# Optimization experiments

Hardware: AMD Instinct MI355X
Metric: run time of the kernel (lower is better)

The kernel has to match this reference:

```python
import math
import jax, jax.numpy as jnp
import numpy as np

B, L, D, H = 4, 2048, 1024, 16
KD = D // H

def setup_inputs() -> dict:
    key = jax.random.key(0)
    k1, k2, k3 = jax.random.split(key, 3)
    x = jax.random.normal(k1, (B, L, D), dtype=jnp.float32)
    pad_mask = jnp.zeros((B, L), dtype=bool)  # True = padded (masked) key position
    w_qkv = jax.random.normal(k2, (D, 3 * D), dtype=jnp.float32) / math.sqrt(D)
    w_out = jax.random.normal(k3, (D, D), dtype=jnp.float32) / math.sqrt(D)
    return {"x": x, "pad_mask": pad_mask, "w_qkv": w_qkv, "w_out": w_out}

def reference(x, pad_mask, w_qkv, w_out):
    Bx, Lx, Dx = x.shape
    qkv = jnp.einsum('bld,de->ble', x, w_qkv)          # [B,L,3D]
    q, k, v = jnp.split(qkv, 3, axis=-1)
    def heads(t):
        return t.reshape(Bx, Lx, H, KD).transpose(0, 2, 1, 3)  # [B,H,L,kd]
    qh, kh, vh = heads(q), heads(k), heads(v)
    scores = jnp.einsum('bhqd,bhkd->bhqk', qh, kh) / math.sqrt(KD)
    causal = jnp.triu(jnp.ones((Lx, Lx), dtype=bool), k=1)[None, None]   # [1,1,L,L]
    mask = causal | pad_mask[:, None, None, :]                            # [B,1,L,L]
    scores = jnp.where(mask, -jnp.inf, scores)
    probs = jax.nn.softmax(scores, axis=-1)
    att = jnp.einsum('bhqk,bhkd->bhqd', probs, vh)
    concat = att.transpose(0, 2, 1, 3).reshape(Bx, Lx, Dx)
    return jnp.einsum('bld,de->ble', concat, w_out)
```

## Files before the change

### kernel.cpp

```cpp
#include <hip/hip_runtime.h>
#include <hip/hip_bf16.h>
#include <math.h>


typedef __bf16 bf16x8 __attribute__((ext_vector_type(8)));
typedef float f32x4 __attribute__((ext_vector_type(4)));

__device__ __forceinline__ f32x4 mfma16(bf16x8 a, bf16x8 b, f32x4 c) {
    return __builtin_amdgcn_mfma_f32_16x16x32_bf16(a, b, c, 0, 0, 0);
}

__device__ __forceinline__ void async16(const void* g, void* l) {
    __builtin_amdgcn_global_load_lds(
        (const __attribute__((address_space(1))) unsigned int*)g,
        (__attribute__((address_space(3))) unsigned int*)l, 16, 0, 0);
}

__global__ void prologue(const float* __restrict__ x,
                         __hip_bfloat16* __restrict__ xb,
                         const float* __restrict__ w0,
                         __hip_bfloat16* __restrict__ t0,
                         const float* __restrict__ w1,
                         __hip_bfloat16* __restrict__ t1) {
    __shared__ float tile[32][33];
    int bid = blockIdx.x, tid = threadIdx.x;
    if (bid < 8192) {
        int i = bid * 256 + tid;
        float4 v = ((const float4*)x)[i];
        __hip_bfloat16 t[4];
        t[0] = __float2bfloat16(v.x);
        t[1] = __float2bfloat16(v.y);
        t[2] = __float2bfloat16(v.z);
        t[3] = __float2bfloat16(v.w);
        ((uint2*)xb)[i] = *(uint2*)t;
        return;
    }
    int t = bid - 8192;
    const float* W;
    __hip_bfloat16* Wt;
    int N, bx, by;
    if (t < 3072) { W = w0; Wt = t0; N = 3072; bx = t % 96; by = t / 96; }
    else { t -= 3072; W = w1; Wt = t1; N = 1024; bx = t % 32; by = t / 32; }
    const int K = 1024;
    int tx = tid & 31, ty = tid >> 5;
    int n0 = bx * 32, k0 = by * 32;
#pragma unroll
    for (int i = 0; i < 4; ++i)
        tile[ty + 8 * i][tx] = W[(size_t)(k0 + ty + 8 * i) * N + n0 + tx];
    __syncthreads();
#pragma unroll
    for (int i = 0; i < 4; ++i)
        Wt[(size_t)(n0 + ty + 8 * i) * K + k0 + tx] =
            __float2bfloat16(tile[tx][ty + 8 * i]);
}

__global__ __launch_bounds__(256) void gemm_qkv(
    const __hip_bfloat16* __restrict__ A, const __hip_bfloat16* __restrict__ Bt,
    __hip_bfloat16* __restrict__ Qo, __hip_bfloat16* __restrict__ Ko,
    __hip_bfloat16* __restrict__ Vto, int M, int N, int K) {
    __shared__ __hip_bfloat16 As[128 * 64];
    __shared__ __hip_bfloat16 Bs[128 * 64];
    int tid = threadIdx.x;
    int wave = tid >> 6, lane = tid & 63;
    int quad = lane >> 4, l16 = lane & 15;
    int m0 = blockIdx.x * 128, n0 = blockIdx.y * 128;
    int wm = (wave >> 1) * 64, wn = (wave & 1) * 64;
    int srow = lane >> 3;
    int g8 = ((lane & 7) ^ srow) * 8;
    int swz = (l16 & 7);
    f32x4 acc[4][4] = {};
    for (int k0 = 0; k0 < K; k0 += 64) {
        __syncthreads();
#pragma unroll
        for (int j = 0; j < 4; ++j) {
            int r0 = (j * 4 + wave) * 8;
            async16(&A[(size_t)(m0 + r0 + srow) * K + k0 + g8], &As[r0 * 64]);
            async16(&Bt[(size_t)(n0 + r0 + srow) * K + k0 + g8], &Bs[r0 * 64]);
        }
        __syncthreads();
        bf16x8 af[2][4], bfr[2][4];
#pragma unroll
        for (int c = 0; c < 2; ++c) {
            int pg = ((c * 4 + quad) ^ swz) * 8;
#pragma unroll
            for (int i = 0; i < 4; ++i) {
                af[c][i]  = *(const bf16x8*)&As[(wm + i * 16 + l16) * 64 + pg];
                bfr[c][i] = *(const bf16x8*)&Bs[(wn + i * 16 + l16) * 64 + pg];
            }
        }
#pragma unroll
        for (int c = 0; c < 2; ++c)
#pragma unroll
            for (int mi = 0; mi < 4; ++mi)
#pragma unroll
                for (int ni = 0; ni < 4; ++ni)
                    acc[mi][ni] = mfma16(af[c][mi], bfr[c][ni], acc[mi][ni]);
    }
#pragma unroll
    for (int mi = 0; mi < 4; ++mi) {
#pragma unroll
        for (int ni = 0; ni < 4; ++ni) {
            int row0 = m0 + wm + mi * 16 + quad * 4;
            int col = n0 + wn + ni * 16 + l16;
            int which = col >> 10, hd = col & 1023;
            int h = hd >> 6, d = hd & 63;
            if (which == 0) {
#pragma unroll
                for (int r = 0; r < 4; ++r) {
                    int row = row0 + r;
                    int b = row >> 11, l = row & 2047;
                    Qo[(((size_t)b * 16 + h) * 2048 + l) * 64 + d] =
                        __float2bfloat16(acc[mi][ni][r] * 0.18033688011f);
                }
            } else if (which == 1) {
#pragma unroll
                for (int r = 0; r < 4; ++r) {
                    int row = row0 + r;
                    int b = row >> 11, l = row & 2047;
                    Ko[(((size_t)b * 16 + h) * 2048 + l) * 64 + d] =
                        __float2bfloat16(acc[mi][ni][r]);
                }
            } else {
                int b = row0 >> 11, l = row0 & 2047;
                __hip_bfloat16 t4[4];
#pragma unroll
                for (int r = 0; r < 4; ++r)
                    t4[r] = __float2bfloat16(acc[mi][ni][r]);
                *(uint2*)&Vto[(((size_t)b * 16 + h) * 64 + d) * 2048 + l] =
                    *(uint2*)t4;
            }
        }
    }
}

__global__ __launch_bounds__(256) void gemm_out(
    const __hip_bfloat16* __restrict__ A, const __hip_bfloat16* __restrict__ Bt,
    float* __restrict__ Cf, int M, int N, int K) {
    __shared__ __hip_bfloat16 As[2][128 * 64];
    __shared__ __hip_bfloat16 Bs[2][64 * 64];
    int tid = threadIdx.x;
    int wave = tid >> 6, lane = tid & 63;
    int quad = lane >> 4, l16 = lane & 15;
    int m0 = blockIdx.x * 128, n0 = blockIdx.y * 64;
    int wm = wave * 32;
    int srow = lane >> 3;
    int g8 = ((lane & 7) ^ srow) * 8;
    int swz = (l16 & 7);

    auto stage = [&](int k0, int buf) {
#pragma unroll
        for (int j = 0; j < 4; ++j) {
            int r0 = (wave * 4 + j) * 8;
            async16(&A[(size_t)(m0 + r0 + srow) * K + k0 + g8],
                    &As[buf][r0 * 64]);
        }
#pragma unroll
        for (int j = 0; j < 2; ++j) {
            int r0 = (wave * 2 + j) * 8;
            async16(&Bt[(size_t)(n0 + r0 + srow) * K + k0 + g8],
                    &Bs[buf][r0 * 64]);
        }
    };

    f32x4 acc[2][4] = {};
    int niter = K >> 6;
    stage(0, 0);
    for (int kt = 0; kt < niter; ++kt) {
        int cur = kt & 1;
        __syncthreads();
        if (kt + 1 < niter) stage((kt + 1) * 64, cur ^ 1);
        bf16x8 af[2][2], bfr[2][4];
#pragma unroll
        for (int c = 0; c < 2; ++c) {
            int pg = ((c * 4 + quad) ^ swz) * 8;
#pragma unroll
            for (int i = 0; i < 2; ++i)
                af[c][i] =
                    *(const bf16x8*)&As[cur][(wm + i * 16 + l16) * 64 + pg];
#pragma unroll
            for (int i = 0; i < 4; ++i)
                bfr[c][i] = *(const bf16x8*)&Bs[cur][(i * 16 + l16) * 64 + pg];
        }
#pragma unroll
        for (int c = 0; c < 2; ++c)
#pragma unroll
            for (int mi = 0; mi < 2; ++mi)
#pragma unroll
                for (int ni = 0; ni < 4; ++ni)
                    acc[mi][ni] = mfma16(af[c][mi], bfr[c][ni], acc[mi][ni]);
    }
#pragma unroll
    for (int mi = 0; mi < 2; ++mi)
#pragma unroll
        for (int ni = 0; ni < 4; ++ni) {
            int row0 = m0 + wm + mi * 16 + quad * 4;
            int col = n0 + ni * 16 + l16;
#pragma unroll
            for (int r = 0; r < 4; ++r)
                Cf[(size_t)(row0 + r) * N + col] = acc[mi][ni][r];
        }
}

__global__ __launch_bounds__(256, 2) void attn_kernel(
    const __hip_bfloat16* __restrict__ Q, const __hip_bfloat16* __restrict__ Kk,
    const __hip_bfloat16* __restrict__ Vt,
    const unsigned char* __restrict__ pm, __hip_bfloat16* __restrict__ Ao) {
    __shared__ __hip_bfloat16 Ks[2 * 64 * 64];
    __shared__ __hip_bfloat16 Vs[2 * 64 * 64];
    constexpr int LDK = 72;
    __shared__ __hip_bfloat16 Ps[4 * 32 * LDK];
    __shared__ unsigned char pmS[2048];
    __shared__ unsigned char pmAny[32];
    int tid = threadIdx.x;
    int wave = tid >> 6, lane = tid & 63;
    int quad = lane >> 4, l16 = lane & 15;
    int srow = lane >> 3;
    int g8 = ((lane & 7) ^ srow) * 8;
    int swz = (l16 & 7);
    int lin = blockIdx.x;
    int bh = (lin & 7) * 8 + ((lin >> 3) & 7);
    int pr = lin >> 6;
    int b = bh >> 4, h = bh & 15;
    const __hip_bfloat16* Qbh = Q + (size_t)bh * 2048 * 64;
    const __hip_bfloat16* Kbh = Kk + (size_t)bh * 2048 * 64;
    const __hip_bfloat16* Vbh = Vt + (size_t)bh * 64 * 2048;
    *(uint2*)&pmS[tid * 8] = *(const uint2*)&pm[b * 2048 + tid * 8];
    __syncthreads();
    if (tid < 32) {
        const unsigned long long* q8 = (const unsigned long long*)&pmS[tid * 64];
        unsigned long long v = q8[0] | q8[1] | q8[2] | q8[3] | q8[4] | q8[5] |
                               q8[6] | q8[7];
        pmAny[tid] = v ? 1 : 0;
    }
    __hip_bfloat16* Pw = Ps + wave * 32 * LDK;

    auto stage = [&](int kt, int buf) {
#pragma unroll
        for (int j = 0; j < 2; ++j) {
            int r0 = (j * 4 + wave) * 8;
            async16(&Kbh[((size_t)kt * 64 + r0 + srow) * 64 + g8],
                    &Ks[buf * 4096 + r0 * 64]);
            async16(&Vbh[(size_t)(r0 + srow) * 2048 + kt * 64 + g8],
                    &Vs[buf * 4096 + r0 * 64]);
        }
    };

#pragma unroll
    for (int ph = 0; ph < 2; ++ph) {
        int qt = ph ? pr : 15 - pr;
        int q0 = qt * 128;
        bf16x8 qf[2][2];
#pragma unroll
        for (int mi = 0; mi < 2; ++mi) {
            int qrow = q0 + (wave * 2 + mi) * 16 + l16;
            qf[mi][0] = *(const bf16x8*)&Qbh[(size_t)qrow * 64 + quad * 8];
            qf[mi][1] = *(const bf16x8*)&Qbh[(size_t)qrow * 64 + 32 + quad * 8];
        }
        f32x4 ov[2][4] = {};
        float lacc[2] = {};
        int ktmax = 2 * qt + 1;
        stage(0, 0);
        for (int kt = 0; kt <= ktmax; ++kt) {
            int cur = kt & 1;
            __syncthreads();
            if (kt < ktmax) stage(kt + 1, cur ^ 1);
            const __hip_bfloat16* Kc = &Ks[cur * 4096];
            const __hip_bfloat16* Vc = &Vs[cur * 4096];
            bool anyp = pmAny[kt] != 0;
            bool diag = (kt >= 2 * qt);
            float pv[2][4][4];
#pragma unroll
            for (int kn = 0; kn < 4; ++kn) {
                int krow = (kn * 16 + l16) * 64;
                bf16x8 kf0 = *(const bf16x8*)&Kc[krow + ((quad ^ swz) * 8)];
                bf16x8 kf1 = *(const bf16x8*)&Kc[krow + (((4 + quad) ^ swz) * 8)];
#pragma unroll
                for (int mi = 0; mi < 2; ++mi) {
                    f32x4 s = {};
                    s = mfma16(kf0, qf[mi][0], s);
                    s = mfma16(kf1, qf[mi][1], s);
#pragma unroll
                    for (int r = 0; r < 4; ++r)
                        pv[mi][kn][r] = __builtin_amdgcn_exp2f(s[r]);
                }
            }
            if (anyp) {
#pragma unroll
                for (int kn = 0; kn < 4; ++kn)
#pragma unroll
                    for (int r = 0; r < 4; ++r) {
                        bool pmk = pmS[kt * 64 + kn * 16 + quad * 4 + r] != 0;
#pragma unroll
                        for (int mi = 0; mi < 2; ++mi)
                            if (pmk) pv[mi][kn][r] = 0.f;
                    }
            }
            if (diag) {
#pragma unroll
                for (int mi = 0; mi < 2; ++mi) {
                    int qv = q0 + (wave * 2 + mi) * 16 + l16;
#pragma unroll
                    for (int kn = 0; kn < 4; ++kn) {
                        int key = kt * 64 + kn * 16 + quad * 4;
#pragma unroll
                        for (int r = 0; r < 4; ++r)
                            if (key + r > qv) pv[mi][kn][r] = 0.f;
                    }
                }
            }
#pragma unroll
            for (int mi = 0; mi < 2; ++mi) {
#pragma unroll
                for (int kn = 0; kn < 4; ++kn) {
                    lacc[mi] += (pv[mi][kn][0] + pv[mi][kn][1]) +
                                (pv[mi][kn][2] + pv[mi][kn][3]);
                    __hip_bfloat162 lo =
                        __float22bfloat162_rn({pv[mi][kn][0], pv[mi][kn][1]});
                    __hip_bfloat162 hi =
                        __float22bfloat162_rn({pv[mi][kn][2], pv[mi][kn][3]});
                    uint2 w;
                    w.x = *(unsigned int*)&lo;
                    w.y = *(unsigned int*)&hi;
                    *(uint2*)&Pw[(mi * 16 + l16) * LDK + kn * 16 + quad * 4] = w;
                }
            }
#pragma unroll
            for (int mi = 0; mi < 2; ++mi) {
#pragma unroll
                for (int hk = 0; hk < 2; ++hk) {
                    bf16x8 pf = *(const bf16x8*)&Pw[(mi * 16 + l16) * LDK +
                                                    hk * 32 + quad * 8];
#pragma unroll
                    for (int ni = 0; ni < 4; ++ni) {
                        int vrow = (ni * 16 + l16) * 64;
                        bf16x8 vf = *(const bf16x8*)&Vc[vrow +
                                                        (((hk * 4 + quad) ^ swz) *
                                                         8)];
                        ov[mi][ni] = mfma16(vf, pf, ov[mi][ni]);
                    }
                }
            }
        }
#pragma unroll
        for (int mi = 0; mi < 2; ++mi) {
            float rs = lacc[mi];
            rs += __shfl_xor(rs, 16);
            rs += __shfl_xor(rs, 32);
            float inv = 1.0f / rs;
            int qv = q0 + (wave * 2 + mi) * 16 + l16;
            size_t obase = (size_t)(b * 2048 + qv) * 1024 + h * 64;
#pragma unroll
            for (int ni = 0; ni < 4; ++ni) {
                __hip_bfloat162 lo = __float22bfloat162_rn(
                    {ov[mi][ni][0] * inv, ov[mi][ni][1] * inv});
                __hip_bfloat162 hi = __float22bfloat162_rn(
                    {ov[mi][ni][2] * inv, ov[mi][ni][3] * inv});
                uint2 w;
                w.x = *(unsigned int*)&lo;
                w.y = *(unsigned int*)&hi;
                *(uint2*)&Ao[obase + ni * 16 + quad * 4] = w;
            }
        }
        lacc[0] = lacc[1] = 0.f;
    }
}

extern "C" void kernel_launch(void* const* d_in, const int* in_sizes, int n_in,
                              void* d_out, int out_size, void* d_ws,
                              size_t ws_size, hipStream_t stream) {
    (void)in_sizes; (void)n_in; (void)out_size; (void)ws_size;
    const float* x = (const float*)d_in[0];
    const unsigned char* pm = (const unsigned char*)d_in[1];
    const float* wqkv = (const float*)d_in[2];
    const float* wout = (const float*)d_in[3];
    float* out = (float*)d_out;

    char* p = (char*)d_ws;
    auto alloc = [&](size_t bytes) {
        char* q = p;
        p += (bytes + 255) & ~(size_t)255;
        return q;
    };
    __hip_bfloat16* xb    = (__hip_bfloat16*)alloc((size_t)8192 * 1024 * 2);
    __hip_bfloat16* wqkvT = (__hip_bfloat16*)alloc((size_t)3072 * 1024 * 2);
    __hip_bfloat16* woutT = (__hip_bfloat16*)alloc((size_t)1024 * 1024 * 2);
    __hip_bfloat16* qws   = (__hip_bfloat16*)alloc((size_t)8192 * 1024 * 2);
    __hip_bfloat16* kws   = (__hip_bfloat16*)alloc((size_t)8192 * 1024 * 2);
    __hip_bfloat16* vtws  = (__hip_bfloat16*)alloc((size_t)8192 * 1024 * 2);
    __hip_bfloat16* attb  = (__hip_bfloat16*)alloc((size_t)8192 * 1024 * 2);

    prologue<<<8192 + 3072 + 1024, 256, 0, stream>>>(x, xb, wqkv, wqkvT, wout,
                                                     woutT);
    gemm_qkv<<<dim3(64, 24), 256, 0, stream>>>(xb, wqkvT, qws, kws, vtws, 8192,
                                               3072, 1024);
    attn_kernel<<<512, 256, 0, stream>>>(qws, kws, vtws, pm, attb);
    gemm_out<<<dim3(64, 16), 256, 0, stream>>>(attb, woutT, out, 8192, 1024,
                                               1024);
}
```

Measured before the change: 240.1 us.

## Split-K the output projection with 128x128 tiles and vectorize input conversion

The output projection GEMM now uses 128x128 block tiles with a 2x2 wave layout. K is split in two along a z grid dimension: one half writes into the output and the other into a scratch buffer that reuses the Q/K workspace. A separate reduce_add kernel then sums the two partials. The double-buffered async staging is replaced by a single-buffered load/sync/compute loop. Separately, the fp32-to-bf16 conversion of x now handles 8 elements per thread with 16-byte stores, halving its block count. The split adds an extra 32MB partial write plus a full read-modify-write pass over the output, and drops load/compute overlap.

```diff
diff --git a/kernel.cpp b/kernel.cpp
--- a/kernel.cpp
+++ b/kernel.cpp
@@ -24,18 +24,19 @@
                          __hip_bfloat16* __restrict__ t1) {
     __shared__ float tile[32][33];
     int bid = blockIdx.x, tid = threadIdx.x;
-    if (bid < 8192) {
+    if (bid < 4096) {
         int i = bid * 256 + tid;
-        float4 v = ((const float4*)x)[i];
-        __hip_bfloat16 t[4];
-        t[0] = __float2bfloat16(v.x);
-        t[1] = __float2bfloat16(v.y);
-        t[2] = __float2bfloat16(v.z);
-        t[3] = __float2bfloat16(v.w);
-        ((uint2*)xb)[i] = *(uint2*)t;
+        float4 v0 = ((const float4*)x)[2 * i];
+        float4 v1 = ((const float4*)x)[2 * i + 1];
+        __hip_bfloat16 t[8];
+        t[0] = __float2bfloat16(v0.x); t[1] = __float2bfloat16(v0.y);
+        t[2] = __float2bfloat16(v0.z); t[3] = __float2bfloat16(v0.w);
+        t[4] = __float2bfloat16(v1.x); t[5] = __float2bfloat16(v1.y);
+        t[6] = __float2bfloat16(v1.z); t[7] = __float2bfloat16(v1.w);
+        ((uint4*)xb)[i] = *(uint4*)t;
         return;
     }
-    int t = bid - 8192;
+    int t = bid - 4096;
     const float* W;
     __hip_bfloat16* Wt;
     int N, bx, by;
@@ -133,72 +134,69 @@
     }
 }
 
-__global__ __launch_bounds__(256) void gemm_out(
+__global__ __launch_bounds__(256) void gemm_out_ks(
     const __hip_bfloat16* __restrict__ A, const __hip_bfloat16* __restrict__ Bt,
-    float* __restrict__ Cf, int M, int N, int K) {
-    __shared__ __hip_bfloat16 As[2][128 * 64];
-    __shared__ __hip_bfloat16 Bs[2][64 * 64];
+    float* __restrict__ C0, float* __restrict__ C1, int M, int N, int K) {
+    __shared__ __hip_bfloat16 As[128 * 64];
+    __shared__ __hip_bfloat16 Bs[128 * 64];
     int tid = threadIdx.x;
     int wave = tid >> 6, lane = tid & 63;
     int quad = lane >> 4, l16 = lane & 15;
-    int m0 = blockIdx.x * 128, n0 = blockIdx.y * 64;
-    int wm = wave * 32;
+    int m0 = blockIdx.x * 128, n0 = blockIdx.y * 128;
+    int wm = (wave >> 1) * 64, wn = (wave & 1) * 64;
     int srow = lane >> 3;
     int g8 = ((lane & 7) ^ srow) * 8;
     int swz = (l16 & 7);
-
-    auto stage = [&](int k0, int buf) {
+    int kh = K >> 1;
+    int kbeg = blockIdx.z * kh, kend = kbeg + kh;
+    float* Cf = blockIdx.z ? C1 : C0;
+    f32x4 acc[4][4] = {};
+    for (int k0 = kbeg; k0 < kend; k0 += 64) {
+        __syncthreads();
 #pragma unroll
         for (int j = 0; j < 4; ++j) {
-            int r0 = (wave * 4 + j) * 8;
-            async16(&A[(size_t)(m0 + r0 + srow) * K + k0 + g8],
-                    &As[buf][r0 * 64]);
-        }
-#pragma unroll
-        for (int j = 0; j < 2; ++j) {
-            int r0 = (wave * 2 + j) * 8;
-            async16(&Bt[(size_t)(n0 + r0 + srow) * K + k0 + g8],
-                    &Bs[buf][r0 * 64]);
-        }
-    };
-
-    f32x4 acc[2][4] = {};
-    int niter = K >> 6;
-    stage(0, 0);
-    for (int kt = 0; kt < niter; ++kt) {
-        int cur = kt & 1;
+            int r0 = (j * 4 + wave) * 8;
+            async16(&A[(size_t)(m0 + r0 + srow) * K + k0 + g8], &As[r0 * 64]);
+            async16(&Bt[(size_t)(n0 + r0 + srow) * K + k0 + g8], &Bs[r0 * 64]);
+        }
         __syncthreads();
-        if (kt + 1 < niter) stage((kt + 1) * 64, cur ^ 1);
-        bf16x8 af[2][2], bfr[2][4];
+        bf16x8 af[2][4], bfr[2][4];
 #pragma unroll
         for (int c = 0; c < 2; ++c) {
             int pg = ((c * 4 + quad) ^ swz) * 8;
 #pragma unroll
-            for (int i = 0; i < 2; ++i)
-                af[c][i] =
-                    *(const bf16x8*)&As[cur][(wm + i * 16 + l16) * 64 + pg];
-#pragma unroll
-            for (int i = 0; i < 4; ++i)
-                bfr[c][i] = *(const bf16x8*)&Bs[cur][(i * 16 + l16) * 64 + pg];
+            for (int i = 0; i < 4; ++i) {
+                af[c][i]  = *(const bf16x8*)&As[(wm + i * 16 + l16) * 64 + pg];
+                bfr[c][i] = *(const bf16x8*)&Bs[(wn + i * 16 + l16) * 64 + pg];
+            }
         }
 #pragma unroll
         for (int c = 0; c < 2; ++c)
 #pragma unroll
-            for (int mi = 0; mi < 2; ++mi)
+            for (int mi = 0; mi < 4; ++mi)
 #pragma unroll
                 for (int ni = 0; ni < 4; ++ni)
                     acc[mi][ni] = mfma16(af[c][mi], bfr[c][ni], acc[mi][ni]);
     }
 #pragma unroll
-    for (int mi = 0; mi < 2; ++mi)
+    for (int mi = 0; mi < 4; ++mi)
 #pragma unroll
         for (int ni = 0; ni < 4; ++ni) {
             int row0 = m0 + wm + mi * 16 + quad * 4;
-            int col = n0 + ni * 16 + l16;
+            int col = n0 + wn + ni * 16 + l16;
 #pragma unroll
             for (int r = 0; r < 4; ++r)
                 Cf[(size_t)(row0 + r) * N + col] = acc[mi][ni][r];
         }
+}
+
+__global__ void reduce_add(float* __restrict__ out,
+                           const float* __restrict__ p1) {
+    int i = blockIdx.x * 256 + threadIdx.x;
+    float4 a = ((const float4*)out)[i];
+    float4 b = ((const float4*)p1)[i];
+    a.x += b.x; a.y += b.y; a.z += b.z; a.w += b.w;
+    ((float4*)out)[i] = a;
 }
 
 __global__ __launch_bounds__(256, 2) void attn_kernel(
@@ -388,12 +386,14 @@
     __hip_bfloat16* kws   = (__hip_bfloat16*)alloc((size_t)8192 * 1024 * 2);
     __hip_bfloat16* vtws  = (__hip_bfloat16*)alloc((size_t)8192 * 1024 * 2);
     __hip_bfloat16* attb  = (__hip_bfloat16*)alloc((size_t)8192 * 1024 * 2);
-
-    prologue<<<8192 + 3072 + 1024, 256, 0, stream>>>(x, xb, wqkv, wqkvT, wout,
+    float* part1 = (float*)qws;
+
+    prologue<<<4096 + 3072 + 1024, 256, 0, stream>>>(x, xb, wqkv, wqkvT, wout,
                                                      woutT);
     gemm_qkv<<<dim3(64, 24), 256, 0, stream>>>(xb, wqkvT, qws, kws, vtws, 8192,
                                                3072, 1024);
     attn_kernel<<<512, 256, 0, stream>>>(qws, kws, vtws, pm, attb);
-    gemm_out<<<dim3(64, 16), 256, 0, stream>>>(attb, woutT, out, 8192, 1024,
-                                               1024);
-}
+    gemm_out_ks<<<dim3(64, 8, 2), 256, 0, stream>>>(attb, woutT, out, part1,
+                                                    8192, 1024, 1024);
+    reduce_add<<<8192, 256, 0, stream>>>(out, part1);
+}
```

Result: slower. 249.5 us (+3.9%).
